# Optimization experiments

Hardware: AMD Instinct MI355X
Metric: run time of the kernel (lower is better)

Reference implementation:

```python
import jax, jax.numpy as jnp
import numpy as np

B, Z, H, TC, TD, DOUT = 128, 512, 512, 16, 16, 176
DIN_DEC = DOUT + H  # 688: concat(prev_note, conductor_embedding)


def setup_inputs() -> dict:
    key = jax.random.key(0)
    ks = jax.random.split(key, 24)

    def glorot(k, shape):
        lim = np.sqrt(6.0 / (shape[0] + shape[1]))
        return jax.random.uniform(k, shape, jnp.float32, -lim, lim)

    return {
        'z_ssm_embedding': jax.random.normal(ks[0], (B, Z), jnp.float32),
        'pianoroll': jax.random.uniform(ks[1], (B, TC * TD, DOUT), jnp.float32),
        'ssm': jax.random.uniform(ks[2], (B, TC * TD, TC * TD), jnp.float32),
        # z -> conductor initial states (h1,c1,h2,c2), tanh dense
        'Wz': glorot(ks[3], (Z, 4 * H)), 'bz': jnp.zeros((4 * H,), jnp.float32),
        # conductor 2-layer LSTM (input 512)
        'cond_W1': glorot(ks[4], (H, 4 * H)), 'cond_U1': glorot(ks[5], (H, 4 * H)), 'cond_b1': jnp.zeros((4 * H,), jnp.float32),
        'cond_W2': glorot(ks[6], (H, 4 * H)), 'cond_U2': glorot(ks[7], (H, 4 * H)), 'cond_b2': jnp.zeros((4 * H,), jnp.float32),
        # conductor embedding -> decoder initial states, tanh dense
        'Wcd': glorot(ks[8], (H, 4 * H)), 'bcd': jnp.zeros((4 * H,), jnp.float32),
        # core decoder 2-layer LSTM (input 688)
        'dec_W1': glorot(ks[9], (DIN_DEC, 4 * H)), 'dec_U1': glorot(ks[10], (H, 4 * H)), 'dec_b1': jnp.zeros((4 * H,), jnp.float32),
        'dec_W2': glorot(ks[11], (H, 4 * H)), 'dec_U2': glorot(ks[12], (H, 4 * H)), 'dec_b2': jnp.zeros((4 * H,), jnp.float32),
        # output projection (softmax)
        'Wp': glorot(ks[13], (H, DOUT)), 'bp': jnp.zeros((DOUT,), jnp.float32),
    }


def _lstm_step(x, h, c, W, U, b):
    g = x @ W + h @ U + b  # (B, 4H), keras gate order i,f,g,o
    i, f, gg, o = jnp.split(g, 4, axis=-1)
    c = jax.nn.sigmoid(f) * c + jax.nn.sigmoid(i) * jnp.tanh(gg)
    h = jax.nn.sigmoid(o) * jnp.tanh(c)
    return h, c


def reference(z_ssm_embedding, pianoroll, ssm,
              Wz, bz,
              cond_W1, cond_U1, cond_b1, cond_W2, cond_U2, cond_b2,
              Wcd, bcd,
              dec_W1, dec_U1, dec_b1, dec_W2, dec_U2, dec_b2,
              Wp, bp):
    b = z_ssm_embedding.shape[0]
    # conductor initial states from latent (tanh dense, split per layer h/c)
    s = jnp.tanh(z_ssm_embedding @ Wz + bz)
    ch1, cc1, ch2, cc2 = jnp.split(s, 4, axis=-1)
    # In the source, conductor_input and conductor_states are never updated
    # across the outer loop, so the conductor embedding is identical for all
    # 16 segments: compute the single step once.
    x0 = jnp.zeros((b, H), jnp.float32)
    h1, _ = _lstm_step(x0, ch1, cc1, cond_W1, cond_U1, cond_b1)
    cond_emb, _ = _lstm_step(h1, ch2, cc2, cond_W2, cond_U2, cond_b2)  # (B, H)
    # decoder initial states from conductor embedding (same for all segments)
    sd = jnp.tanh(cond_emb @ Wcd + bcd)
    dh1, dc1, dh2, dc2 = jnp.split(sd, 4, axis=-1)

    def seg(note_prev, _):
        def step(carry, _):
            h1, c1, h2, c2, note = carry
            x = jnp.concatenate([note, cond_emb], axis=-1)  # (B, 688)
            h1, c1 = _lstm_step(x, h1, c1, dec_W1, dec_U1, dec_b1)
            h2, c2 = _lstm_step(h1, h2, c2, dec_W2, dec_U2, dec_b2)
            note = jax.nn.softmax(h2 @ Wp + bp, axis=-1)  # output projection
            return (h1, c1, h2, c2, note), note
        (_, _, _, _, note_last), notes = jax.lax.scan(
            step, (dh1, dc1, dh2, dc2, note_prev), None, length=TD)
        return note_last, notes  # notes: (TD, B, DOUT)

    note0 = jnp.zeros((b, DOUT), jnp.float32)
    _, all_notes = jax.lax.scan(seg, note0, None, length=TC)  # (TC, TD, B, DOUT)
    return all_notes.reshape(TC * TD, b, DOUT).transpose(1, 0, 2)  # (B, 256, 176)
```

## Files before the change

kernel.cpp:

```cpp
#include <hip/hip_runtime.h>
#include <hip/hip_bf16.h>
#include <math.h>

#define Bn    128
#define NGn   2048
#define TTn   256
#define DOn   176
#define NBLK  256
#define NTHR  1024
#define HPAR  65536
#define ACC_PAR 24576

typedef unsigned int uint;
typedef unsigned long long u64;
using f32x4 = __attribute__((ext_vector_type(4))) float;
using s16x8 = __attribute__((ext_vector_type(8))) short;
union FR { uint u[4]; s16x8 s; };

struct KA {
  const float *z,*Wz,*bz,*cU1,*cb1,*cW2,*cU2,*cb2,*Wcd,*bcd;
  const float *dW1,*dU1,*db1,*dW2,*dU2,*db2,*Wp,*bp;
  float *zT,*sT,*ggate,*h1cT,*ceT,*sdT,*beffP,*db1P,*db2P,*WEp,*out;
  uint *WAh,*WAl,*WBh,*WBl,*h1pk,*h2pk,*dh1pk,*dh2pk;
  int  *accI;
};

__device__ unsigned g_cnt_l1[16 * 32];
__device__ unsigned g_cnt;
__device__ unsigned g_gen;
__device__ unsigned pod_ctr[8 * 64];

__device__ __forceinline__ float sigm(float x) { return 1.0f / (1.0f + __expf(-x)); }

__device__ __forceinline__ float aloadF(const float* p) {
  return __hip_atomic_load(p, __ATOMIC_RELAXED, __HIP_MEMORY_SCOPE_AGENT);
}
__device__ __forceinline__ void astoreF(float* p, float v) {
  __hip_atomic_store(p, v, __ATOMIC_RELAXED, __HIP_MEMORY_SCOPE_AGENT);
}
__device__ __forceinline__ uint aloadU(const uint* p) {
  return __hip_atomic_load(p, __ATOMIC_RELAXED, __HIP_MEMORY_SCOPE_AGENT);
}
__device__ __forceinline__ void astoreU(uint* p, uint v) {
  __hip_atomic_store(p, v, __ATOMIC_RELAXED, __HIP_MEMORY_SCOPE_AGENT);
}
__device__ __forceinline__ int aloadI(const int* p) {
  return __hip_atomic_load(p, __ATOMIC_RELAXED, __HIP_MEMORY_SCOPE_AGENT);
}
__device__ __forceinline__ u64 aload64(const u64* p) {
  return __hip_atomic_load(p, __ATOMIC_RELAXED, __HIP_MEMORY_SCOPE_AGENT);
}

__device__ __forceinline__ void split2(float v, unsigned short& h, unsigned short& l) {
  __hip_bfloat16 bh = __float2bfloat16(v);
  float hf = __bfloat162float(bh);
  __hip_bfloat16 bl = __float2bfloat16(v - hf);
  h = *(unsigned short*)&bh; l = *(unsigned short*)&bl;
}
__device__ __forceinline__ uint packsplit(float v) {
  unsigned short h, l; split2(v, h, l);
  return (uint)h | ((uint)l << 16);
}

__device__ __forceinline__ void gbar() {
  __syncthreads();
  if (threadIdx.x == 0) {
    asm volatile("s_waitcnt vmcnt(0)" ::: "memory");
    unsigned g0 = __hip_atomic_load(&g_gen, __ATOMIC_RELAXED, __HIP_MEMORY_SCOPE_AGENT);
    unsigned p1 = __hip_atomic_fetch_add(&g_cnt_l1[(blockIdx.x >> 4) * 32], 1u,
                                         __ATOMIC_RELAXED, __HIP_MEMORY_SCOPE_AGENT);
    if (p1 == 15u) {
      unsigned p2 = __hip_atomic_fetch_add(&g_cnt, 1u, __ATOMIC_RELAXED, __HIP_MEMORY_SCOPE_AGENT);
      if (p2 == 15u) {
        #pragma unroll
        for (int i = 0; i < 16; i++)
          __hip_atomic_store(&g_cnt_l1[i * 32], 0u, __ATOMIC_RELAXED, __HIP_MEMORY_SCOPE_AGENT);
        __hip_atomic_store(&g_cnt, 0u, __ATOMIC_RELAXED, __HIP_MEMORY_SCOPE_AGENT);
        asm volatile("s_waitcnt vmcnt(0)" ::: "memory");
        __hip_atomic_fetch_add(&g_gen, 1u, __ATOMIC_RELAXED, __HIP_MEMORY_SCOPE_AGENT);
      }
    }
    while (__hip_atomic_load(&g_gen, __ATOMIC_RELAXED, __HIP_MEMORY_SCOPE_AGENT) == g0)
      __builtin_amdgcn_s_sleep(1);
  }
  __syncthreads();
}

__device__ __forceinline__ void pbar2(int pod, unsigned& tgt) {
  __syncthreads();
  if (threadIdx.x == 0) {
    asm volatile("s_waitcnt vmcnt(0)" ::: "memory");
    unsigned* ctr = &pod_ctr[pod * 64];
    __hip_atomic_fetch_add(ctr, 1u, __ATOMIC_RELAXED, __HIP_MEMORY_SCOPE_AGENT);
    while ((int)(__hip_atomic_load(ctr, __ATOMIC_RELAXED, __HIP_MEMORY_SCOPE_AGENT) - tgt) < 0) { }
  }
  __syncthreads();
  tgt += 32;
}

__device__ __forceinline__ void stageN(float* __restrict__ xs, const float* __restrict__ X,
                                       int nrows, int b0, int tid) {
  for (int i = tid; i < nrows * 16; i += NTHR)
    xs[i] = aloadF(X + (size_t)(i >> 4) * Bn + b0 + (i & 15));
}

template<int KC>
__device__ __forceinline__ void gemm16(const float* __restrict__ Wb, int colbase,
                                       int kq, int cg, int bg,
                                       const float* __restrict__ xsrc, float acc[16]) {
  const float* wp = Wb + (size_t)(kq * KC) * NGn + colbase + cg * 4;
  const float* xp = xsrc + (kq * KC) * 16 + bg * 4;
  #pragma unroll 2
  for (int kk = 0; kk < KC; kk++) {
    const float4 w4 = *(const float4*)(wp);
    const float4 x4 = *(const float4*)(xp);
    acc[0]  = fmaf(w4.x, x4.x, acc[0]);  acc[1]  = fmaf(w4.x, x4.y, acc[1]);
    acc[2]  = fmaf(w4.x, x4.z, acc[2]);  acc[3]  = fmaf(w4.x, x4.w, acc[3]);
    acc[4]  = fmaf(w4.y, x4.x, acc[4]);  acc[5]  = fmaf(w4.y, x4.y, acc[5]);
    acc[6]  = fmaf(w4.y, x4.z, acc[6]);  acc[7]  = fmaf(w4.y, x4.w, acc[7]);
    acc[8]  = fmaf(w4.z, x4.x, acc[8]);  acc[9]  = fmaf(w4.z, x4.y, acc[9]);
    acc[10] = fmaf(w4.z, x4.z, acc[10]); acc[11] = fmaf(w4.z, x4.w, acc[11]);
    acc[12] = fmaf(w4.w, x4.x, acc[12]); acc[13] = fmaf(w4.w, x4.y, acc[13]);
    acc[14] = fmaf(w4.w, x4.z, acc[14]); acc[15] = fmaf(w4.w, x4.w, acc[15]);
    wp += NGn; xp += 16;
  }
}

__device__ __forceinline__ void pstore(float* __restrict__ part, int kq, int cg, int bg,
                                       const float acc[16]) {
  #pragma unroll
  for (int c = 0; c < 4; c++) {
    float* p = part + (size_t)(kq * 64 + cg * 4 + c) * 17 + bg * 4;
    *(float4*)p = make_float4(acc[c*4], acc[c*4+1], acc[c*4+2], acc[c*4+3]);
  }
}

template<int MODE>
__device__ __forceinline__ void epi_plain(const float* bias, float* out,
                                          int colbase, int b0, int tid,
                                          const float* __restrict__ part) {
  int cl = tid >> 4, bl = tid & 15;
  float s = 0.0f;
  #pragma unroll
  for (int w = 0; w < 8; w++) s += part[(w * 64 + cl) * 17 + bl];
  if (bias) s += bias[colbase + cl];
  if (MODE == 0) s = tanhf(s);
  astoreF(out + (size_t)(colbase + cl) * Bn + b0 + bl, s);
}

__device__ __forceinline__ void cond_nl(const float* gb, const float* cbias,
                                        const float* cin, float* hout, int bid, int tid) {
  int i = bid * NTHR + tid;
  if (i < 512 * Bn) {
    int hid = i >> 7, b = i & 127;
    float gi = aloadF(gb + (size_t)hid * Bn + b)            + cbias[hid];
    float gf = aloadF(gb + (size_t)(512 + hid) * Bn + b)    + cbias[512 + hid];
    float gg = aloadF(gb + (size_t)(1024 + hid) * Bn + b)   + cbias[1024 + hid];
    float go = aloadF(gb + (size_t)(1536 + hid) * Bn + b)   + cbias[1536 + hid];
    float cprev = aloadF(cin + (size_t)hid * Bn + b);
    float c = sigm(gf) * cprev + sigm(gi) * tanhf(gg);
    astoreF(hout + (size_t)hid * Bn + b, sigm(go) * tanhf(c));
  }
}

__device__ __forceinline__ void unpack64(const u64* d, FR& xh, FR& xl) {
  #pragma unroll
  for (int q = 0; q < 4; q++) {
    uint lo = (uint)d[q], hi = (uint)(d[q] >> 32);
    xh.u[q] = (lo & 0xffffu) | (hi << 16);
    xl.u[q] = (lo >> 16) | (hi & 0xffff0000u);
  }
}
__device__ __forceinline__ void unpackU8(uint4 a, uint4 b, FR& xh, FR& xl) {
  xh.u[0] = (a.x & 0xffffu) | (a.y << 16); xl.u[0] = (a.x >> 16) | (a.y & 0xffff0000u);
  xh.u[1] = (a.z & 0xffffu) | (a.w << 16); xl.u[1] = (a.z >> 16) | (a.w & 0xffff0000u);
  xh.u[2] = (b.x & 0xffffu) | (b.y << 16); xl.u[2] = (b.x >> 16) | (b.y & 0xffff0000u);
  xh.u[3] = (b.z & 0xffffu) | (b.w << 16); xl.u[3] = (b.z >> 16) | (b.w & 0xffff0000u);
}

struct MC {
  const uint *WAh,*WAl,*WBh,*WBl,*dh1pk,*dh2pk;
  uint *h1pk,*h2pk;
  const float *beffP,*db2P,*Wp,*bp;
  int *accI;
  float *out;
  uint *NTu;
  float *plog,*gbuf,*cst,*h2s;
  int j, b0;
};

#define MFMA3(ACC, XH, XL, WH, WL)                                            \
  ACC = __builtin_amdgcn_mfma_f32_16x16x32_bf16(XH.s, WH.s, ACC, 0, 0, 0);    \
  ACC = __builtin_amdgcn_mfma_f32_16x16x32_bf16(XL.s, WH.s, ACC, 0, 0, 0);    \
  ACC = __builtin_amdgcn_mfma_f32_16x16x32_bf16(XH.s, WL.s, ACC, 0, 0, 0);

__device__ __forceinline__ void doKS(const uint* WH, const uint* WL, int ks, int lane,
                                     const FR& xh, const FR& xl, f32x4 acc[4]) {
  #pragma unroll
  for (int nt = 0; nt < 4; nt++) {
    FR wh, wl;
    *(uint4*)wh.u = *(const uint4*)(WH + (ks * 4 + nt) * 256 + lane * 4);
    *(uint4*)wl.u = *(const uint4*)(WL + (ks * 4 + nt) * 256 + lane * 4);
    MFMA3(acc[nt], xh, xl, wh, wl)
  }
}

__device__ __forceinline__ void wrplog(const MC& c, int wid, int lane, const f32x4 acc[4]) {
  #pragma unroll
  for (int nt = 0; nt < 4; nt++)
    #pragma unroll
    for (int r = 0; r < 4; r++)
      c.plog[((wid * 4 + nt) * 4 + r) * 68 + lane] = acc[nt][r];
}

__device__ __forceinline__ void reduce16(const MC& c, int tid, const float* biasv) {
  int cl = tid >> 4, bl = tid & 15;
  float s = 0.f;
  #pragma unroll
  for (int k2 = 0; k2 < 16; k2++)
    s += c.plog[((k2 * 4 + (cl >> 4)) * 4 + (bl & 3)) * 68 + (bl >> 2) * 16 + (cl & 15)];
  c.gbuf[cl * 16 + bl] = s + biasv[cl * 16 + bl];
}

__device__ __forceinline__ void phaseA(const MC& c, int t, bool doLSTM,
                                       float* __restrict__ beffL) {
  const int tid = threadIdx.x, wid = tid >> 6, lane = tid & 63;
  const int m = lane & 15, kh = lane >> 4;
  const int par = t & 1; const bool rst = (t & 15) == 0;
  if (t > 0) {
    const int wv = wid;
    const int* ai = c.accI + ((par ^ 1) * ACC_PAR) + wv * 192;
    float lg[3], pv[3];
    #pragma unroll
    for (int rep = 0; rep < 3; rep++) {
      int o = lane + rep * 64;
      lg[rep] = (o < DOn) ? (float)aloadI(ai + o) * (1.0f / 1048576.0f) + c.bp[o] : -1e30f;
    }
    float mx = fmaxf(fmaxf(lg[0], lg[1]), lg[2]);
    #pragma unroll
    for (int d = 1; d < 64; d <<= 1) mx = fmaxf(mx, __shfl_xor(mx, d));
    float sum = 0.f;
    #pragma unroll
    for (int rep = 0; rep < 3; rep++) {
      int o = lane + rep * 64;
      pv[rep] = (o < DOn) ? __expf(lg[rep] - mx) : 0.f;
      sum += pv[rep];
    }
    #pragma unroll
    for (int d = 1; d < 64; d <<= 1) sum += __shfl_xor(sum, d);
    const float inv = 1.0f / sum;
    #pragma unroll
    for (int rep = 0; rep < 3; rep++) {
      int o = lane + rep * 64;
      float p = pv[rep] * inv;
      c.NTu[((o >> 3) * 16 + wv) * 8 + (o & 7)] = (o < DOn) ? packsplit(p) : 0u;
      if (c.j < 16 && wv == c.j && o < DOn)
        c.out[((size_t)(c.b0 + c.j) * TTn + (t - 1)) * DOn + o] = p;
    }
  }
  __syncthreads();
  if (!doLSTM) return;
  const uint* WH = c.WAh + (size_t)c.j * 22528;
  const uint* WL = c.WAl + (size_t)c.j * 22528;
  const uint* hsrc = rst ? c.dh1pk : (c.h1pk + (par ^ 1) * HPAR);
  f32x4 acc[4] = {{0,0,0,0},{0,0,0,0},{0,0,0,0},{0,0,0,0}};
  if (wid < 3) {
    #pragma unroll
    for (int i = 0; i < 2; i++) {
      const int ks = wid * 2 + i;
      const uint* p = c.NTu + ((ks * 4 + kh) * 16 + m) * 8;
      uint4 a = *(const uint4*)p, b = *(const uint4*)(p + 4);
      FR xh, xl; unpackU8(a, b, xh, xl);
      doKS(WH, WL, ks, lane, xh, xl, acc);
    }
  } else if (wid < 6) {
    u64 xr[8];
    #pragma unroll
    for (int i = 0; i < 2; i++) {
      const int ks = wid * 2 + i;
      const u64* p = (const u64*)hsrc + ((size_t)(((ks - 6) * 4 + kh) * 128 + c.b0 + m)) * 4;
      #pragma unroll
      for (int q = 0; q < 4; q++) xr[i * 4 + q] = aload64(p + q);
    }
    #pragma unroll
    for (int i = 0; i < 2; i++) {
      FR xh, xl; unpack64(&xr[i * 4], xh, xl);
      doKS(WH, WL, wid * 2 + i, lane, xh, xl, acc);
    }
  } else {
    u64 xr[4];
    const u64* p = (const u64*)hsrc + ((size_t)((wid * 4 + kh) * 128 + c.b0 + m)) * 4;
    #pragma unroll
    for (int q = 0; q < 4; q++) xr[q] = aload64(p + q);
    FR xh, xl; unpack64(xr, xh, xl);
    doKS(WH, WL, 12 + (wid - 6), lane, xh, xl, acc);
  }
  wrplog(c, wid, lane, acc);
  __syncthreads();
  reduce16(c, tid, beffL);
  __syncthreads();
  if (tid < 256) {
    int h = tid >> 4, bl = tid & 15;
    float gi = c.gbuf[(h*4+0)*16+bl], gf = c.gbuf[(h*4+1)*16+bl];
    float gg = c.gbuf[(h*4+2)*16+bl], go = c.gbuf[(h*4+3)*16+bl];
    float cp = rst ? c.cst[512 + tid] : c.cst[tid];
    float cc = sigm(gf) * cp + sigm(gi) * tanhf(gg);
    c.cst[tid] = cc;
    astoreU(c.h1pk + par * HPAR
              + ((size_t)((c.j * 2 + (h >> 3)) * 128 + c.b0 + bl)) * 8 + (h & 7),
            packsplit(sigm(go) * tanhf(cc)));
  }
}

__device__ __forceinline__ void phaseB(const MC& c, int t, float* __restrict__ db2L) {
  const int tid = threadIdx.x, wid = tid >> 6, lane = tid & 63;
  const int m = lane & 15, kh = lane >> 4;
  const int par = t & 1; const bool rst = (t & 15) == 0;
  const uint* s1 = c.h1pk + par * HPAR;
  const uint* s2 = rst ? c.dh2pk : (c.h2pk + (par ^ 1) * HPAR);
  const uint* WH = c.WBh + (size_t)c.j * 32768;
  const uint* WL = c.WBl + (size_t)c.j * 32768;
  u64 xr[8];
  #pragma unroll
  for (int i = 0; i < 2; i++) {
    const int ks = wid * 2 + i;
    const uint* sp = (ks < 16) ? s1 : s2;
    const u64* p = (const u64*)sp + ((size_t)(((ks & 15) * 4 + kh) * 128 + c.b0 + m)) * 4;
    #pragma unroll
    for (int q = 0; q < 4; q++) xr[i * 4 + q] = aload64(p + q);
  }
  f32x4 acc[4] = {{0,0,0,0},{0,0,0,0},{0,0,0,0},{0,0,0,0}};
  #pragma unroll
  for (int i = 0; i < 2; i++) {
    FR xh, xl; unpack64(&xr[i * 4], xh, xl);
    doKS(WH, WL, wid * 2 + i, lane, xh, xl, acc);
  }
  wrplog(c, wid, lane, acc);
  __syncthreads();
  reduce16(c, tid, db2L);
  __syncthreads();
  if (tid < 256) {
    int h = tid >> 4, bl = tid & 15;
    float gi = c.gbuf[(h*4+0)*16+bl], gf = c.gbuf[(h*4+1)*16+bl];
    float gg = c.gbuf[(h*4+2)*16+bl], go = c.gbuf[(h*4+3)*16+bl];
    float cp = rst ? c.cst[768 + tid] : c.cst[256 + tid];
    float cc = sigm(gf) * cp + sigm(gi) * tanhf(gg);
    c.cst[256 + tid] = cc;
    float h2v = sigm(go) * tanhf(cc);
    c.h2s[h * 16 + bl] = h2v;
    astoreU(c.h2pk + par * HPAR
              + ((size_t)((c.j * 2 + (h >> 3)) * 128 + c.b0 + bl)) * 8 + (h & 7),
            packsplit(h2v));
  }
  __syncthreads();
  const int o = tid & 255, q = tid >> 8;
  if (o < DOn) {
    float wv[16];
    #pragma unroll
    for (int h = 0; h < 16; h++) wv[h] = c.Wp[(size_t)(c.j * 16 + h) * DOn + o];
    #pragma unroll
    for (int rep = 0; rep < 4; rep++) {
      const int bl = q * 4 + rep;
      float s = 0.f;
      #pragma unroll
      for (int h = 0; h < 16; h++) s = fmaf(c.h2s[h * 16 + bl], wv[h], s);
      __hip_atomic_fetch_add(c.accI + par * ACC_PAR + bl * 192 + o,
                             __float2int_rn(s * 1048576.0f),
                             __ATOMIC_RELAXED, __HIP_MEMORY_SCOPE_AGENT);
    }
  }
  if (tid < 96)
    astoreU((uint*)(c.accI + (par ^ 1) * ACC_PAR + c.j * 96 + tid), 0u);
}

__global__ void __launch_bounds__(NTHR, 1)
hd_kernel(KA A) {
  __shared__ float buf[25088];
  __shared__ float beffL[1024], db2L[1024];
  float* xs = buf;
  float* part = buf + 16384;
  const int bid = blockIdx.x, tid = threadIdx.x;
  const int lane = tid & 63;
  const int kqP = tid >> 6, cgP = lane & 15, bgP = lane >> 4;
  const int rP = bid & 31, btP = bid >> 5;
  const int htP = (rP & 7) * 4 + (rP >> 3);
  const int colbaseP = htP * 64, b0P = btP * 16;
  const int pod = bid >> 5;

  unsigned tgt = __hip_atomic_load(&pod_ctr[pod * 64], __ATOMIC_RELAXED,
                                   __HIP_MEMORY_SCOPE_AGENT) + 32;

  {
    const int i0 = bid * NTHR + tid;
    if (i0 < 512 * Bn) { int zb = i0 >> 9, zk = i0 & 511; astoreF(A.zT + (size_t)zk * Bn + zb, A.z[i0]); }
    if (i0 < NGn) {
      int hid = i0 >> 2, g = i0 & 3, sc = g * 512 + hid;
      astoreF(A.db1P + i0, A.db1[sc]);
      astoreF(A.db2P + i0, A.db2[sc]);
    }
    if (i0 < 2 * ACC_PAR) astoreU((uint*)(A.accI + i0), 0u);
    for (int i = i0; i < 512 * NGn; i += NBLK * NTHR) {
      int k = i >> 11, pc = i & 2047;
      int hid = pc >> 2, g = pc & 3;
      astoreF(A.WEp + i, A.dW1[(size_t)(176 + k) * NGn + g * 512 + hid]);
    }
    for (int i = i0; i < 720896; i += NBLK * NTHR) {
      int col = i & 2047, kp = i >> 11, k = kp * 2;
      float w0, w1;
      if (k < 176)      { w0 = A.dW1[(size_t)k * NGn + col];       w1 = A.dW1[(size_t)(k + 1) * NGn + col]; }
      else if (k < 192) { w0 = 0.f; w1 = 0.f; }
      else              { w0 = A.dU1[(size_t)(k - 192) * NGn + col]; w1 = A.dU1[(size_t)(k - 191) * NGn + col]; }
      unsigned short h0, l0, h1, l1; split2(w0, h0, l0); split2(w1, h1, l1);
      int g = col >> 9, hid = col & 511;
      int jj = hid >> 4, cl = (hid & 15) * 4 + g;
      int nt = cl >> 4, n = cl & 15;
      int ks = k >> 5, kr = k & 31, lh = kr >> 3, q = (kr >> 1) & 3;
      int idx = ((jj * 22 + ks) * 4 + nt) * 256 + (lh * 16 + n) * 4 + q;
      astoreU(A.WAh + idx, (uint)h0 | ((uint)h1 << 16));
      astoreU(A.WAl + idx, (uint)l0 | ((uint)l1 << 16));
    }
  }
  gbar();
  {
    stageN(xs, A.zT, 512, b0P, tid); __syncthreads();
    if (tid < 512) {
      float acc[16] = {0,0,0,0,0,0,0,0,0,0,0,0,0,0,0,0};
      gemm16<64>(A.Wz, colbaseP, kqP, cgP, bgP, xs, acc);
      pstore(part, kqP, cgP, bgP, acc);
    }
    __syncthreads();
    epi_plain<0>(A.bz, A.sT, colbaseP, b0P, tid, part);
  }
  gbar();
  {
    stageN(xs, A.sT, 512, b0P, tid); __syncthreads();
    if (tid < 512) {
      float acc[16] = {0,0,0,0,0,0,0,0,0,0,0,0,0,0,0,0};
      gemm16<64>(A.cU1, colbaseP, kqP, cgP, bgP, xs, acc);
      pstore(part, kqP, cgP, bgP, acc);
    }
    __syncthreads();
    epi_plain<1>(nullptr, A.ggate, colbaseP, b0P, tid, part);
  }
  gbar();
  cond_nl(A.ggate, A.cb1, A.sT + (size_t)512 * Bn, A.h1cT, bid, tid);
  gbar();
  {
    stageN(xs, A.h1cT, 512, b0P, tid);
    stageN(xs + 8192, A.sT + (size_t)1024 * Bn, 512, b0P, tid);
    __syncthreads();
    if (tid < 512) {
      float acc[16] = {0,0,0,0,0,0,0,0,0,0,0,0,0,0,0,0};
      gemm16<64>(A.cW2, colbaseP, kqP, cgP, bgP, xs, acc);
      gemm16<64>(A.cU2, colbaseP, kqP, cgP, bgP, xs + 8192, acc);
      pstore(part, kqP, cgP, bgP, acc);
    }
    __syncthreads();
    epi_plain<1>(nullptr, A.ggate, colbaseP, b0P, tid, part);
  }
  gbar();
  cond_nl(A.ggate, A.cb2, A.sT + (size_t)1536 * Bn, A.ceT, bid, tid);
  gbar();
  {
    stageN(xs, A.ceT, 512, b0P, tid); __syncthreads();
    if (tid < 512) {
      float acc[16] = {0,0,0,0,0,0,0,0,0,0,0,0,0,0,0,0};
      gemm16<64>(A.Wcd, colbaseP, kqP, cgP, bgP, xs, acc);
      pstore(part, kqP, cgP, bgP, acc);
    }
    __syncthreads();
    epi_plain<0>(A.bcd, A.sdT, colbaseP, b0P, tid, part);
    __syncthreads();
    if (tid < 512) {
      float acc[16] = {0,0,0,0,0,0,0,0,0,0,0,0,0,0,0,0};
      gemm16<64>(A.WEp, colbaseP, kqP, cgP, bgP, xs, acc);
      pstore(part, kqP, cgP, bgP, acc);
    }
    __syncthreads();
    epi_plain<1>(A.db1P, A.beffP, colbaseP, b0P, tid, part);
  }
  gbar();
  {
    const int i0 = bid * NTHR + tid;
    for (int i = i0; i < 1048576; i += NBLK * NTHR) {
      int col = i & 2047, kp = i >> 11, k = kp * 2;
      float w0, w1;
      if (k < 512) { w0 = A.dW2[(size_t)k * NGn + col];         w1 = A.dW2[(size_t)(k + 1) * NGn + col]; }
      else         { w0 = A.dU2[(size_t)(k - 512) * NGn + col]; w1 = A.dU2[(size_t)(k - 511) * NGn + col]; }
      unsigned short h0, l0, h1, l1; split2(w0, h0, l0); split2(w1, h1, l1);
      int g = col >> 9, hid = col & 511;
      int jj = hid >> 4, cl = (hid & 15) * 4 + g;
      int nt = cl >> 4, n = cl & 15;
      int ks = k >> 5, kr = k & 31, lh = kr >> 3, q = (kr >> 1) & 3;
      int idx = ((jj * 32 + ks) * 4 + nt) * 256 + (lh * 16 + n) * 4 + q;
      astoreU(A.WBh + idx, (uint)h0 | ((uint)h1 << 16));
      astoreU(A.WBl + idx, (uint)l0 | ((uint)l1 << 16));
    }
    if (i0 < 512 * Bn) {
      int hid = i0 >> 7, b = i0 & 127;
      astoreU(A.dh1pk + ((size_t)((hid >> 3) * 128 + b)) * 8 + (hid & 7),
              packsplit(aloadF(A.sdT + (size_t)hid * Bn + b)));
      astoreU(A.dh2pk + ((size_t)((hid >> 3) * 128 + b)) * 8 + (hid & 7),
              packsplit(aloadF(A.sdT + (size_t)(1024 + hid) * Bn + b)));
    }
  }
  gbar();

  MC c;
  c.WAh = A.WAh; c.WAl = A.WAl; c.WBh = A.WBh; c.WBl = A.WBl;
  c.dh1pk = A.dh1pk; c.dh2pk = A.dh2pk;
  c.h1pk = A.h1pk; c.h2pk = A.h2pk;
  c.beffP = A.beffP; c.db2P = A.db2P; c.Wp = A.Wp; c.bp = A.bp; c.out = A.out;
  c.accI = A.accI + pod * 3072;
  c.NTu = (uint*)buf;
  c.plog = buf + 3072;
  c.gbuf = buf + 20480;
  c.cst  = buf + 21504;
  c.h2s  = buf + 22528;
  c.j = bid & 31;
  c.b0 = pod * 16;
  if (tid < 256) {
    int h = tid >> 4, bl = tid & 15;
    c.cst[512 + tid] = aloadF(A.sdT + (size_t)(512 + c.j * 16 + h) * Bn + c.b0 + bl);
    c.cst[768 + tid] = aloadF(A.sdT + (size_t)(1536 + c.j * 16 + h) * Bn + c.b0 + bl);
  }
  {
    int cl = tid >> 4, bl = tid & 15;
    beffL[tid] = aloadF(A.beffP + (size_t)(c.j * 64 + cl) * Bn + c.b0 + bl);
    db2L[tid] = A.db2P[c.j * 64 + cl];
  }
  for (int i = tid; i < 3072; i += NTHR) c.NTu[i] = 0u;
  __syncthreads();

  for (int t = 0; t < TTn; t++) {
    phaseA(c, t, true, beffL);
    pbar2(pod, tgt);
    phaseB(c, t, db2L);
    pbar2(pod, tgt);
  }
  phaseA(c, TTn, false, beffL);
}

extern "C" void kernel_launch(void* const* d_in, const int* in_sizes, int n_in,
                              void* d_out, int out_size, void* d_ws, size_t ws_size,
                              hipStream_t stream) {
  (void)in_sizes; (void)n_in; (void)out_size; (void)ws_size;
  KA a;
  a.z   = (const float*)d_in[0];
  a.Wz  = (const float*)d_in[3];  a.bz  = (const float*)d_in[4];
  a.cU1 = (const float*)d_in[6];  a.cb1 = (const float*)d_in[7];
  a.cW2 = (const float*)d_in[8];  a.cU2 = (const float*)d_in[9];  a.cb2 = (const float*)d_in[10];
  a.Wcd = (const float*)d_in[11]; a.bcd = (const float*)d_in[12];
  a.dW1 = (const float*)d_in[13]; a.dU1 = (const float*)d_in[14]; a.db1 = (const float*)d_in[15];
  a.dW2 = (const float*)d_in[16]; a.dU2 = (const float*)d_in[17]; a.db2 = (const float*)d_in[18];
  a.Wp  = (const float*)d_in[19]; a.bp  = (const float*)d_in[20];

  float* ws = (float*)d_ws;
  size_t off = 0;
  a.zT    = ws + off; off += (size_t)512  * Bn;
  a.sT    = ws + off; off += (size_t)NGn  * Bn;
  a.ggate = ws + off; off += (size_t)NGn  * Bn;
  a.h1cT  = ws + off; off += (size_t)512  * Bn;
  a.ceT   = ws + off; off += (size_t)512  * Bn;
  a.sdT   = ws + off; off += (size_t)NGn  * Bn;
  a.beffP = ws + off; off += (size_t)NGn  * Bn;
  a.db1P  = ws + off; off += (size_t)NGn;
  a.db2P  = ws + off; off += (size_t)NGn;
  a.WEp   = ws + off; off += (size_t)512 * NGn;
  a.WBh   = (uint*)a.WEp;
  a.WBl   = (uint*)(ws + off); off += (size_t)1048576;
  a.WAh   = (uint*)(ws + off); off += (size_t)720896;
  a.WAl   = (uint*)(ws + off); off += (size_t)720896;
  a.h1pk  = (uint*)(ws + off); off += (size_t)2 * HPAR;
  a.h2pk  = (uint*)(ws + off); off += (size_t)2 * HPAR;
  a.dh1pk = (uint*)(ws + off); off += (size_t)HPAR;
  a.dh2pk = (uint*)(ws + off); off += (size_t)HPAR;
  a.accI  = (int*)(ws + off);  off += (size_t)2 * ACC_PAR;
  a.out   = (float*)d_out;

  hd_kernel<<<dim3(NBLK), dim3(NTHR), 0, stream>>>(a);
}
```

Measured before the change: 7.156 ms.

## Replace pod atomic-counter barrier with per-block slot flags and prefetch hidden states

The pod barrier, where 32 blocks did a fetch_add on one shared counter and then spun on it, becomes a slot-based barrier. Each block stores its generation into its own padded slot, and 32 lanes poll all slots in parallel. This removes atomic contention on a single address. The phase A and phase B functions are merged into one step function. Global loads of the recurrent h1/h2 states and the softmax accumulators are issued before the softmax and the barrier so their latency overlaps other work. The trade-off is more register pressure from the prefetched values held live across phases, and a correctness dependence on the slot generation counters persisting across launches.

Result: faster. 6.942 ms (-3.0%).

```diff
diff --git a/kernel.cpp b/kernel.cpp
--- a/kernel.cpp
+++ b/kernel.cpp
@@ -28,7 +28,7 @@
 __device__ unsigned g_cnt_l1[16 * 32];
 __device__ unsigned g_cnt;
 __device__ unsigned g_gen;
-__device__ unsigned pod_ctr[8 * 64];
+__device__ unsigned pod_slot[8 * 32 * 32];
 
 __device__ __forceinline__ float sigm(float x) { return 1.0f / (1.0f + __expf(-x)); }
 
@@ -86,16 +86,18 @@
   __syncthreads();
 }
 
-__device__ __forceinline__ void pbar2(int pod, unsigned& tgt) {
-  __syncthreads();
-  if (threadIdx.x == 0) {
-    asm volatile("s_waitcnt vmcnt(0)" ::: "memory");
-    unsigned* ctr = &pod_ctr[pod * 64];
-    __hip_atomic_fetch_add(ctr, 1u, __ATOMIC_RELAXED, __HIP_MEMORY_SCOPE_AGENT);
-    while ((int)(__hip_atomic_load(ctr, __ATOMIC_RELAXED, __HIP_MEMORY_SCOPE_AGENT) - tgt) < 0) { }
-  }
-  __syncthreads();
-  tgt += 32;
+__device__ __forceinline__ void pbarS(int pod, int j, unsigned& tgt) {
+  __syncthreads();
+  if (threadIdx.x < 32) {
+    if (threadIdx.x == 0) {
+      asm volatile("s_waitcnt vmcnt(0)" ::: "memory");
+      astoreU(&pod_slot[(pod * 32 + j) * 32], tgt);
+    }
+    const uint* sl = &pod_slot[(pod * 32 + (int)threadIdx.x) * 32];
+    while ((int)(aloadU(sl) - tgt) < 0) { }
+  }
+  __syncthreads();
+  tgt += 1;
 }
 
 __device__ __forceinline__ void stageN(float* __restrict__ xs, const float* __restrict__ X,
@@ -222,80 +224,101 @@
   c.gbuf[cl * 16 + bl] = s + biasv[cl * 16 + bl];
 }
 
-__device__ __forceinline__ void phaseA(const MC& c, int t, bool doLSTM,
-                                       float* __restrict__ beffL) {
+__device__ __forceinline__ void smBody(const MC& c, int t, int wv, int lane,
+                                       int ai0, int ai1, int ai2) {
+  float lg[3], pv[3];
+  const int o0 = lane, o1 = lane + 64, o2 = lane + 128;
+  lg[0] = (o0 < DOn) ? (float)ai0 * (1.0f / 1048576.0f) + c.bp[o0] : -1e30f;
+  lg[1] = (o1 < DOn) ? (float)ai1 * (1.0f / 1048576.0f) + c.bp[o1] : -1e30f;
+  lg[2] = (o2 < DOn) ? (float)ai2 * (1.0f / 1048576.0f) + c.bp[o2] : -1e30f;
+  float mx = fmaxf(fmaxf(lg[0], lg[1]), lg[2]);
+  #pragma unroll
+  for (int d = 1; d < 64; d <<= 1) mx = fmaxf(mx, __shfl_xor(mx, d));
+  float sum = 0.f;
+  #pragma unroll
+  for (int rep = 0; rep < 3; rep++) {
+    int o = lane + rep * 64;
+    pv[rep] = (o < DOn) ? __expf(lg[rep] - mx) : 0.f;
+    sum += pv[rep];
+  }
+  #pragma unroll
+  for (int d = 1; d < 64; d <<= 1) sum += __shfl_xor(sum, d);
+  const float inv = 1.0f / sum;
+  #pragma unroll
+  for (int rep = 0; rep < 3; rep++) {
+    int o = lane + rep * 64;
+    float p = pv[rep] * inv;
+    c.NTu[((o >> 3) * 16 + wv) * 8 + (o & 7)] = (o < DOn) ? packsplit(p) : 0u;
+    if (c.j < 16 && wv == c.j && o < DOn)
+      c.out[((size_t)(c.b0 + c.j) * TTn + (t - 1)) * DOn + o] = p;
+  }
+}
+
+__device__ __forceinline__ void stepFn(const MC& c, int t, const float* beffL,
+                                       const float* db2L, int pod, unsigned& tgt) {
   const int tid = threadIdx.x, wid = tid >> 6, lane = tid & 63;
   const int m = lane & 15, kh = lane >> 4;
   const int par = t & 1; const bool rst = (t & 15) == 0;
+
+  int ai0 = 0, ai1 = 0, ai2 = 0;
   if (t > 0) {
-    const int wv = wid;
-    const int* ai = c.accI + ((par ^ 1) * ACC_PAR) + wv * 192;
-    float lg[3], pv[3];
+    const int* ai = c.accI + ((par ^ 1) * ACC_PAR) + wid * 192 + lane;
+    ai0 = aloadI(ai); ai1 = aloadI(ai + 64); ai2 = aloadI(ai + 128);
+  }
+  u64 xa[8];
+  const uint* hsrcA = rst ? c.dh1pk : (c.h1pk + (par ^ 1) * HPAR);
+  if (wid >= 3 && wid < 6) {
     #pragma unroll
-    for (int rep = 0; rep < 3; rep++) {
-      int o = lane + rep * 64;
-      lg[rep] = (o < DOn) ? (float)aloadI(ai + o) * (1.0f / 1048576.0f) + c.bp[o] : -1e30f;
-    }
-    float mx = fmaxf(fmaxf(lg[0], lg[1]), lg[2]);
+    for (int i = 0; i < 2; i++) {
+      const u64* p = (const u64*)hsrcA
+                   + ((size_t)(((wid * 2 - 6 + i) * 4 + kh) * 128 + c.b0 + m)) * 4;
+      #pragma unroll
+      for (int q = 0; q < 4; q++) xa[i * 4 + q] = aload64(p + q);
+    }
+  } else if (wid >= 6) {
+    const u64* p = (const u64*)hsrcA + ((size_t)((wid * 4 + kh) * 128 + c.b0 + m)) * 4;
     #pragma unroll
-    for (int d = 1; d < 64; d <<= 1) mx = fmaxf(mx, __shfl_xor(mx, d));
-    float sum = 0.f;
-    #pragma unroll
-    for (int rep = 0; rep < 3; rep++) {
-      int o = lane + rep * 64;
-      pv[rep] = (o < DOn) ? __expf(lg[rep] - mx) : 0.f;
-      sum += pv[rep];
-    }
-    #pragma unroll
-    for (int d = 1; d < 64; d <<= 1) sum += __shfl_xor(sum, d);
-    const float inv = 1.0f / sum;
-    #pragma unroll
-    for (int rep = 0; rep < 3; rep++) {
-      int o = lane + rep * 64;
-      float p = pv[rep] * inv;
-      c.NTu[((o >> 3) * 16 + wv) * 8 + (o & 7)] = (o < DOn) ? packsplit(p) : 0u;
-      if (c.j < 16 && wv == c.j && o < DOn)
-        c.out[((size_t)(c.b0 + c.j) * TTn + (t - 1)) * DOn + o] = p;
-    }
-  }
-  __syncthreads();
-  if (!doLSTM) return;
-  const uint* WH = c.WAh + (size_t)c.j * 22528;
-  const uint* WL = c.WAl + (size_t)c.j * 22528;
-  const uint* hsrc = rst ? c.dh1pk : (c.h1pk + (par ^ 1) * HPAR);
-  f32x4 acc[4] = {{0,0,0,0},{0,0,0,0},{0,0,0,0},{0,0,0,0}};
-  if (wid < 3) {
+    for (int q = 0; q < 4; q++) xa[q] = aload64(p + q);
+  }
+  u64 xb[8];
+  if (wid >= 8) {
+    const uint* s2 = rst ? c.dh2pk : (c.h2pk + (par ^ 1) * HPAR);
     #pragma unroll
     for (int i = 0; i < 2; i++) {
       const int ks = wid * 2 + i;
-      const uint* p = c.NTu + ((ks * 4 + kh) * 16 + m) * 8;
-      uint4 a = *(const uint4*)p, b = *(const uint4*)(p + 4);
-      FR xh, xl; unpackU8(a, b, xh, xl);
-      doKS(WH, WL, ks, lane, xh, xl, acc);
-    }
-  } else if (wid < 6) {
-    u64 xr[8];
-    #pragma unroll
-    for (int i = 0; i < 2; i++) {
-      const int ks = wid * 2 + i;
-      const u64* p = (const u64*)hsrc + ((size_t)(((ks - 6) * 4 + kh) * 128 + c.b0 + m)) * 4;
+      const u64* p = (const u64*)s2
+                   + ((size_t)(((ks & 15) * 4 + kh) * 128 + c.b0 + m)) * 4;
       #pragma unroll
-      for (int q = 0; q < 4; q++) xr[i * 4 + q] = aload64(p + q);
-    }
-    #pragma unroll
-    for (int i = 0; i < 2; i++) {
-      FR xh, xl; unpack64(&xr[i * 4], xh, xl);
-      doKS(WH, WL, wid * 2 + i, lane, xh, xl, acc);
-    }
-  } else {
-    u64 xr[4];
-    const u64* p = (const u64*)hsrc + ((size_t)((wid * 4 + kh) * 128 + c.b0 + m)) * 4;
-    #pragma unroll
-    for (int q = 0; q < 4; q++) xr[q] = aload64(p + q);
-    FR xh, xl; unpack64(xr, xh, xl);
-    doKS(WH, WL, 12 + (wid - 6), lane, xh, xl, acc);
-  }
-  wrplog(c, wid, lane, acc);
+      for (int q = 0; q < 4; q++) xb[i * 4 + q] = aload64(p + q);
+    }
+  }
+
+  if (t > 0) smBody(c, t, wid, lane, ai0, ai1, ai2);
+  __syncthreads();
+
+  {
+    const uint* WH = c.WAh + (size_t)c.j * 22528;
+    const uint* WL = c.WAl + (size_t)c.j * 22528;
+    f32x4 acc[4] = {{0,0,0,0},{0,0,0,0},{0,0,0,0},{0,0,0,0}};
+    if (wid < 3) {
+      #pragma unroll
+      for (int i = 0; i < 2; i++) {
+        const int ks = wid * 2 + i;
+        const uint* p = c.NTu + ((ks * 4 + kh) * 16 + m) * 8;
+        uint4 a = *(const uint4*)p, b = *(const uint4*)(p + 4);
+        FR xh, xl; unpackU8(a, b, xh, xl);
+        doKS(WH, WL, ks, lane, xh, xl, acc);
+      }
+    } else if (wid < 6) {
+      FR xh, xl;
+      unpack64(&xa[0], xh, xl); doKS(WH, WL, wid * 2, lane, xh, xl, acc);
+      unpack64(&xa[4], xh, xl); doKS(WH, WL, wid * 2 + 1, lane, xh, xl, acc);
+    } else {
+      FR xh, xl; unpack64(&xa[0], xh, xl);
+      doKS(WH, WL, 12 + (wid - 6), lane, xh, xl, acc);
+    }
+    wrplog(c, wid, lane, acc);
+  }
   __syncthreads();
   reduce16(c, tid, beffL);
   __syncthreads();
@@ -310,32 +333,27 @@
               + ((size_t)((c.j * 2 + (h >> 3)) * 128 + c.b0 + bl)) * 8 + (h & 7),
             packsplit(sigm(go) * tanhf(cc)));
   }
-}
-
-__device__ __forceinline__ void phaseB(const MC& c, int t, float* __restrict__ db2L) {
-  const int tid = threadIdx.x, wid = tid >> 6, lane = tid & 63;
-  const int m = lane & 15, kh = lane >> 4;
-  const int par = t & 1; const bool rst = (t & 15) == 0;
-  const uint* s1 = c.h1pk + par * HPAR;
-  const uint* s2 = rst ? c.dh2pk : (c.h2pk + (par ^ 1) * HPAR);
-  const uint* WH = c.WBh + (size_t)c.j * 32768;
-  const uint* WL = c.WBl + (size_t)c.j * 32768;
-  u64 xr[8];
-  #pragma unroll
-  for (int i = 0; i < 2; i++) {
-    const int ks = wid * 2 + i;
-    const uint* sp = (ks < 16) ? s1 : s2;
-    const u64* p = (const u64*)sp + ((size_t)(((ks & 15) * 4 + kh) * 128 + c.b0 + m)) * 4;
+  pbarS(pod, c.j, tgt);
+
+  if (wid < 8) {
+    const uint* s1 = c.h1pk + par * HPAR;
     #pragma unroll
-    for (int q = 0; q < 4; q++) xr[i * 4 + q] = aload64(p + q);
-  }
-  f32x4 acc[4] = {{0,0,0,0},{0,0,0,0},{0,0,0,0},{0,0,0,0}};
-  #pragma unroll
-  for (int i = 0; i < 2; i++) {
-    FR xh, xl; unpack64(&xr[i * 4], xh, xl);
-    doKS(WH, WL, wid * 2 + i, lane, xh, xl, acc);
-  }
-  wrplog(c, wid, lane, acc);
+    for (int i = 0; i < 2; i++) {
+      const int ks = wid * 2 + i;
+      const u64* p = (const u64*)s1 + ((size_t)((ks * 4 + kh) * 128 + c.b0 + m)) * 4;
+      #pragma unroll
+      for (int q = 0; q < 4; q++) xb[i * 4 + q] = aload64(p + q);
+    }
+  }
+  {
+    const uint* WH = c.WBh + (size_t)c.j * 32768;
+    const uint* WL = c.WBl + (size_t)c.j * 32768;
+    f32x4 acc[4] = {{0,0,0,0},{0,0,0,0},{0,0,0,0},{0,0,0,0}};
+    FR xh, xl;
+    unpack64(&xb[0], xh, xl); doKS(WH, WL, wid * 2, lane, xh, xl, acc);
+    unpack64(&xb[4], xh, xl); doKS(WH, WL, wid * 2 + 1, lane, xh, xl, acc);
+    wrplog(c, wid, lane, acc);
+  }
   __syncthreads();
   reduce16(c, tid, db2L);
   __syncthreads();
@@ -353,24 +371,34 @@
             packsplit(h2v));
   }
   __syncthreads();
-  const int o = tid & 255, q = tid >> 8;
-  if (o < DOn) {
-    float wv[16];
-    #pragma unroll
-    for (int h = 0; h < 16; h++) wv[h] = c.Wp[(size_t)(c.j * 16 + h) * DOn + o];
-    #pragma unroll
-    for (int rep = 0; rep < 4; rep++) {
-      const int bl = q * 4 + rep;
-      float s = 0.f;
+  {
+    const int o = tid & 255, q = tid >> 8;
+    if (o < DOn) {
+      float wv[16];
       #pragma unroll
-      for (int h = 0; h < 16; h++) s = fmaf(c.h2s[h * 16 + bl], wv[h], s);
-      __hip_atomic_fetch_add(c.accI + par * ACC_PAR + bl * 192 + o,
-                             __float2int_rn(s * 1048576.0f),
-                             __ATOMIC_RELAXED, __HIP_MEMORY_SCOPE_AGENT);
-    }
-  }
-  if (tid < 96)
-    astoreU((uint*)(c.accI + (par ^ 1) * ACC_PAR + c.j * 96 + tid), 0u);
+      for (int h = 0; h < 16; h++) wv[h] = c.Wp[(size_t)(c.j * 16 + h) * DOn + o];
+      #pragma unroll
+      for (int rep = 0; rep < 4; rep++) {
+        const int bl = q * 4 + rep;
+        float s = 0.f;
+        #pragma unroll
+        for (int h = 0; h < 16; h++) s = fmaf(c.h2s[h * 16 + bl], wv[h], s);
+        __hip_atomic_fetch_add(c.accI + par * ACC_PAR + bl * 192 + o,
+                               __float2int_rn(s * 1048576.0f),
+                               __ATOMIC_RELAXED, __HIP_MEMORY_SCOPE_AGENT);
+      }
+    }
+    if (tid < 96)
+      astoreU((uint*)(c.accI + (par ^ 1) * ACC_PAR + c.j * 96 + tid), 0u);
+  }
+  pbarS(pod, c.j, tgt);
+}
+
+__device__ __forceinline__ void smTail(const MC& c, int t) {
+  const int tid = threadIdx.x, wid = tid >> 6, lane = tid & 63;
+  const int par = t & 1;
+  const int* ai = c.accI + ((par ^ 1) * ACC_PAR) + wid * 192 + lane;
+  smBody(c, t, wid, lane, aloadI(ai), aloadI(ai + 64), aloadI(ai + 128));
 }
 
 __global__ void __launch_bounds__(NTHR, 1)
@@ -387,8 +415,7 @@
   const int colbaseP = htP * 64, b0P = btP * 16;
   const int pod = bid >> 5;
 
-  unsigned tgt = __hip_atomic_load(&pod_ctr[pod * 64], __ATOMIC_RELAXED,
-                                   __HIP_MEMORY_SCOPE_AGENT) + 32;
+  unsigned tgt = aloadU(&pod_slot[(pod * 32 + (bid & 31)) * 32]) + 1;
 
   {
     const int i0 = bid * NTHR + tid;
@@ -532,13 +559,9 @@
   for (int i = tid; i < 3072; i += NTHR) c.NTu[i] = 0u;
   __syncthreads();
 
-  for (int t = 0; t < TTn; t++) {
-    phaseA(c, t, true, beffL);
-    pbar2(pod, tgt);
-    phaseB(c, t, db2L);
-    pbar2(pod, tgt);
-  }
-  phaseA(c, TTn, false, beffL);
+  for (int t = 0; t < TTn; t++)
+    stepFn(c, t, beffL, db2L, pod, tgt);
+  smTail(c, TTn);
 }
 
 extern "C" void kernel_launch(void* const* d_in, const int* in_sizes, int n_in,
```
